# Performance work log

Measured on AMD Instinct MI355X. Metric: run time of the kernel, lower is better.

Reference implementation:

```python
import jax, jax.numpy as jnp
from jax import lax
import numpy as np

B, T, V, E, H, D, NH = 64, 121, 100000, 300, 256, 512, 3  # D = 2*H (BiLSTM output)


def setup_inputs() -> dict:
    key = jax.random.key(0)
    ks = jax.random.split(key, 24)
    s = 0.05
    n = lambda k, shp: (jax.random.normal(k, shp, dtype=jnp.float32) * s)
    return {
        'tokens': jax.random.randint(ks[0], (B, T), 0, V, dtype=jnp.int32),
        'lengths': jax.random.randint(ks[1], (B,), 1, T + 1, dtype=jnp.int32),
        'emb': n(ks[2], (V, E)),
        'Wx_f': n(ks[3], (E, 4 * H)), 'Wh_f': n(ks[4], (H, 4 * H)), 'b_f': jnp.zeros((4 * H,), jnp.float32),
        'Wx_b': n(ks[5], (E, 4 * H)), 'Wh_b': n(ks[6], (H, 4 * H)), 'b_b': jnp.zeros((4 * H,), jnp.float32),
        'W1': n(ks[7], (4 * D, E)), 'b1': jnp.zeros((E,), jnp.float32),
        'W2': n(ks[8], (E, 1)), 'b2': jnp.zeros((1,), jnp.float32),
        'Wr': n(ks[9], (D, D)), 'Ur': n(ks[10], (D, D)), 'br': jnp.zeros((D,), jnp.float32),
        'Wc': n(ks[11], (D, D)), 'Uc': n(ks[12], (D, D)), 'bc': jnp.zeros((D,), jnp.float32),
        'q': n(ks[13], (B, D)),
        'W_hops': n(ks[14], (NH, 3 * D, D)), 'b_hops': jnp.zeros((NH, D), jnp.float32),
        'Wo': n(ks[15], (2 * D, 1)), 'bo': jnp.zeros((1,), jnp.float32),
    }


def _lstm(x, Wx, Wh, b, reverse=False):
    # x: [B, T, E] -> outputs [B, T, H]
    xp = jnp.einsum('bte,eg->btg', x, Wx) + b  # precompute input projections
    def cell(carry, xt):
        h, c = carry
        g = xt + h @ Wh
        i, f, gg, o = jnp.split(g, 4, axis=-1)
        c = jax.nn.sigmoid(f) * c + jax.nn.sigmoid(i) * jnp.tanh(gg)
        h = jax.nn.sigmoid(o) * jnp.tanh(c)
        return (h, c), h
    h0 = jnp.zeros((x.shape[0], Wh.shape[0]), x.dtype)
    (_, _), ys = lax.scan(cell, (h0, h0), jnp.swapaxes(xp, 0, 1), reverse=reverse)
    return jnp.swapaxes(ys, 0, 1)


def _attention(facts, q, m, mask, W1, b1, W2, b2):
    # facts [B,T,D]; q,m [B,D] -> softmax attention [B,T] (masked by length)
    qe, me = q[:, None, :], m[:, None, :]
    z = jnp.concatenate([facts * qe, facts * me, jnp.abs(facts - qe), jnp.abs(facts - me)], axis=-1)
    h = jnp.tanh(jnp.einsum('btf,fe->bte', z, W1) + b1)
    s = (jnp.einsum('bte,eo->bto', h, W2) + b2)[..., 0]  # [B,T]
    s = jnp.where(mask, s, jnp.float32(-1e9))
    return jax.nn.softmax(s, axis=1)


def _attn_gru(facts, g, Wr, Ur, br, Wc, Uc, bc):
    # attention-gated GRU over time; episode = final state [B,D]
    def cell(h, inp):
        x, gt = inp
        r = jax.nn.sigmoid(x @ Wr + h @ Ur + br)
        hc = jnp.tanh(x @ Wc + r * (h @ Uc) + bc)
        h = gt[:, None] * hc + (1.0 - gt[:, None]) * h
        return h, None
    h0 = jnp.zeros_like(facts[:, 0])
    h, _ = lax.scan(cell, h0, (jnp.swapaxes(facts, 0, 1), g.T))
    return h


def reference(tokens, lengths, emb, Wx_f, Wh_f, b_f, Wx_b, Wh_b, b_b,
              W1, b1, W2, b2, Wr, Ur, br, Wc, Uc, bc, q,
              W_hops, b_hops, Wo, bo):
    x = emb[tokens]  # [B,T,E]
    fwd = _lstm(x, Wx_f, Wh_f, b_f, reverse=False)
    bwd = _lstm(x, Wx_b, Wh_b, b_b, reverse=True)
    facts = jnp.concatenate([fwd, bwd], axis=-1)  # [B,T,D]
    mask = jnp.arange(T)[None, :] < lengths[:, None]
    m = q
    for i in range(NH):  # episodic memory hops (attention weights shared across hops)
        a = _attention(facts, q, m, mask, W1, b1, W2, b2)
        ep = _attn_gru(facts, a, Wr, Ur, br, Wc, Uc, bc)
        m = jax.nn.relu(jnp.concatenate([m, ep, q], axis=1) @ W_hops[i] + b_hops[i])
    out = jax.nn.sigmoid(jnp.concatenate([m, q], axis=1) @ Wo + bo)
    return jnp.squeeze(out, axis=-1)  # [B]
```

## Files before the change

kernel.cpp:

```cpp
#include <hip/hip_runtime.h>

constexpr int B  = 64;
constexpr int T  = 121;
constexpr int E  = 300;
constexpr int Ep = 320;
constexpr int H  = 256;
constexpr int G4 = 1024;
constexpr int D  = 512;
constexpr int NH = 3;
constexpr int BT = B * T;
constexpr int Mp = 7808;

using short8 = __attribute__((ext_vector_type(8))) short;
using f32x4  = __attribute__((ext_vector_type(4))) float;

__device__ __forceinline__ float sigmoidf(float x) { return 1.0f / (1.0f + __expf(-x)); }
__device__ __forceinline__ float tanhf_fast(float x) {
  float e = __expf(2.0f * x);
  return 1.0f - 2.0f / (e + 1.0f);
}
__device__ __forceinline__ unsigned bf16rne(float x) {
  unsigned u = __float_as_uint(x);
  return (u + 0x7fffu + ((u >> 16) & 1u)) >> 16;
}
__device__ __forceinline__ float bf_lo(unsigned u) { return __uint_as_float(u << 16); }
__device__ __forceinline__ float bf_hi(unsigned u) { return __uint_as_float(u & 0xffff0000u); }
__device__ __forceinline__ float bfu(unsigned short u) { return __uint_as_float(((unsigned)u) << 16); }

#if defined(__has_builtin)
#if __has_builtin(__builtin_amdgcn_sdot4)
#define HAS_SDOT4 1
#endif
#if __has_builtin(__builtin_amdgcn_cvt_f32_ubyte0)
#define HAS_UBYTE 1
#endif
#endif
#ifdef HAS_UBYTE
__device__ __forceinline__ float UB0(unsigned u) { return __builtin_amdgcn_cvt_f32_ubyte0(u); }
__device__ __forceinline__ float UB1(unsigned u) { return __builtin_amdgcn_cvt_f32_ubyte1(u); }
__device__ __forceinline__ float UB2(unsigned u) { return __builtin_amdgcn_cvt_f32_ubyte2(u); }
__device__ __forceinline__ float UB3(unsigned u) { return __builtin_amdgcn_cvt_f32_ubyte3(u); }
#else
__device__ __forceinline__ float UB0(unsigned u) { return (float)(u & 0xffu); }
__device__ __forceinline__ float UB1(unsigned u) { return (float)((u >> 8) & 0xffu); }
__device__ __forceinline__ float UB2(unsigned u) { return (float)((u >> 16) & 0xffu); }
__device__ __forceinline__ float UB3(unsigned u) { return (float)((u >> 24) & 0xffu); }
#endif

__global__ void k_pack_lstm(const float* __restrict__ Wh,
                            uint4* __restrict__ PAQ, uint4* __restrict__ PBQ) {
  int idx = blockIdx.x * 256 + threadIdx.x;
  int k4 = idx >> 8, j = idx & 255;
  int k = 4 * k4;
  uint4 a, bq;
  const float* r0 = Wh + (size_t)(k + 0) * G4;
  const float* r1 = Wh + (size_t)(k + 1) * G4;
  const float* r2 = Wh + (size_t)(k + 2) * G4;
  const float* r3 = Wh + (size_t)(k + 3) * G4;
  a.x  = bf16rne(r0[j]) | (bf16rne(r0[j + 256]) << 16);
  a.y  = bf16rne(r1[j]) | (bf16rne(r1[j + 256]) << 16);
  a.z  = bf16rne(r2[j]) | (bf16rne(r2[j + 256]) << 16);
  a.w  = bf16rne(r3[j]) | (bf16rne(r3[j + 256]) << 16);
  bq.x = bf16rne(r0[j + 512]) | (bf16rne(r0[j + 768]) << 16);
  bq.y = bf16rne(r1[j + 512]) | (bf16rne(r1[j + 768]) << 16);
  bq.z = bf16rne(r2[j + 512]) | (bf16rne(r2[j + 768]) << 16);
  bq.w = bf16rne(r3[j + 512]) | (bf16rne(r3[j + 768]) << 16);
  PAQ[idx] = a;
  PBQ[idx] = bq;
}

__global__ void k_packT(const float* __restrict__ W, unsigned short* __restrict__ WT,
                        int Ksrc, int Nsrc, int stride, int Kpad) {
  int idx = blockIdx.x * 256 + threadIdx.x;
  int n = idx / Kpad, k = idx - n * Kpad;
  float v = (k < Ksrc && n < Nsrc) ? W[(size_t)k * stride + n] : 0.0f;
  WT[idx] = (unsigned short)bf16rne(v);
}

__global__ void k_packxrc(const float* xr, const float* xc, unsigned* XRC) {
  size_t i = (size_t)blockIdx.x * 512 + threadIdx.x;
  float r = xr[i], c = xc[i];
  XRC[i] = bf16rne(r) | (bf16rne(c) << 16);
}

__global__ void k_scales(const float* __restrict__ Ur, const float* __restrict__ Uc,
                         unsigned* __restrict__ smax) {
  int i = blockIdx.x * 256 + threadIdx.x;
  unsigned a = __float_as_uint(fabsf(Ur[i]));
  unsigned b = __float_as_uint(fabsf(Uc[i]));
  for (int off = 32; off > 0; off >>= 1) {
    a = max(a, (unsigned)__shfl_xor((int)a, off));
    b = max(b, (unsigned)__shfl_xor((int)b, off));
  }
  if ((threadIdx.x & 63) == 0) {
    atomicMax(&smax[0], a);
    atomicMax(&smax[1], b);
  }
}

#ifdef HAS_SDOT4
__device__ __forceinline__ unsigned pk4(float a, float b, float c, float d, float inv) {
  int qa = __float2int_rn(a * inv), qb = __float2int_rn(b * inv);
  int qc = __float2int_rn(c * inv), qd = __float2int_rn(d * inv);
  return (qa & 0xff) | ((qb & 0xff) << 8) | ((qc & 0xff) << 16) | ((qd & 0xff) << 24);
}
__global__ void k_pack_gru8(const float* __restrict__ Ur, const float* __restrict__ Uc,
                            const unsigned* __restrict__ smax, uint4* __restrict__ UQ8) {
  int idx = blockIdx.x * 256 + threadIdx.x;
  int k8 = idx >> 9, j = idx & 511;
  int k0 = k8 * 8;
  float invr = 127.0f / __uint_as_float(smax[0]);
  float invc = 127.0f / __uint_as_float(smax[1]);
  uint4 o;
  o.x = pk4(Ur[(size_t)(k0 + 0) * D + j], Ur[(size_t)(k0 + 1) * D + j],
            Ur[(size_t)(k0 + 2) * D + j], Ur[(size_t)(k0 + 3) * D + j], invr);
  o.y = pk4(Uc[(size_t)(k0 + 0) * D + j], Uc[(size_t)(k0 + 1) * D + j],
            Uc[(size_t)(k0 + 2) * D + j], Uc[(size_t)(k0 + 3) * D + j], invc);
  o.z = pk4(Ur[(size_t)(k0 + 4) * D + j], Ur[(size_t)(k0 + 5) * D + j],
            Ur[(size_t)(k0 + 6) * D + j], Ur[(size_t)(k0 + 7) * D + j], invr);
  o.w = pk4(Uc[(size_t)(k0 + 4) * D + j], Uc[(size_t)(k0 + 5) * D + j],
            Uc[(size_t)(k0 + 6) * D + j], Uc[(size_t)(k0 + 7) * D + j], invc);
  UQ8[idx] = o;
}
#else
__global__ void k_pack_gru8(const float* __restrict__ Ur, const float* __restrict__ Uc,
                            const unsigned* __restrict__ smax, uint4* __restrict__ UQ8) {
  int idx = blockIdx.x * 256 + threadIdx.x;
  int k8 = idx >> 9, j = idx & 511;
  float invr = 127.0f / __uint_as_float(smax[0]);
  float invc = 127.0f / __uint_as_float(smax[1]);
  unsigned dw[4];
#pragma unroll
  for (int d = 0; d < 4; ++d) {
    int k0 = k8 * 8 + 2 * d;
    unsigned r0 = (unsigned)(__float2int_rn(Ur[(size_t)k0 * D + j] * invr) + 128);
    unsigned c0 = (unsigned)(__float2int_rn(Uc[(size_t)k0 * D + j] * invc) + 128);
    unsigned r1 = (unsigned)(__float2int_rn(Ur[(size_t)(k0 + 1) * D + j] * invr) + 128);
    unsigned c1 = (unsigned)(__float2int_rn(Uc[(size_t)(k0 + 1) * D + j] * invc) + 128);
    dw[d] = r0 | (c0 << 8) | (r1 << 16) | (c1 << 24);
  }
  UQ8[idx] = make_uint4(dw[0], dw[1], dw[2], dw[3]);
}
#endif

__global__ void k_gather(const int* __restrict__ tokens, const float* __restrict__ emb,
                         unsigned short* __restrict__ xh) {
  int bt = blockIdx.x;
  int tok = tokens[bt];
  const float* src = emb + (size_t)tok * E;
  unsigned short* dst = xh + (size_t)bt * Ep;
  for (int e = threadIdx.x; e < Ep; e += 256)
    dst[e] = (e < E) ? (unsigned short)bf16rne(src[e]) : (unsigned short)0;
}

__global__ __launch_bounds__(256) void k_gemm_mfma(
    const unsigned short* __restrict__ A1, const unsigned short* __restrict__ B1, int K1, int lda1,
    const unsigned short* __restrict__ A2, const unsigned short* __restrict__ B2, int K2, int lda2,
    const float* __restrict__ bias, const float* __restrict__ Cin,
    float* __restrict__ C, int Nreal, int Cstride)
{
  __shared__ unsigned short As[128][40];
  __shared__ unsigned short Bs[64][40];
  int tid = threadIdx.x;
  int l = tid & 63, w = tid >> 6;
  int row0 = blockIdx.y * 128, col0 = blockIdx.x * 64;
  int lrow = l & 15, lk = (l >> 4) * 8, lq = (l >> 4) * 4;
  int ar = tid >> 1, asg = (tid & 1) * 16;
  int br = tid >> 2, bsg = (tid & 3) * 8;
  f32x4 acc[2][4] = {};
#pragma unroll 1
  for (int pass = 0; pass < 2; ++pass) {
    const unsigned short* A  = pass ? A2 : A1;
    const unsigned short* Bt = pass ? B2 : B1;
    int K   = pass ? K2 : K1;
    int lda = pass ? lda2 : lda1;
    if (K == 0) break;
    for (int k0 = 0; k0 < K; k0 += 32) {
      const uint4* ga = (const uint4*)(A + (size_t)(row0 + ar) * lda + k0 + asg);
      uint4 a0 = ga[0], a1 = ga[1];
      uint4 b0 = *(const uint4*)(Bt + (size_t)(col0 + br) * K + k0 + bsg);
      __syncthreads();
      *(uint4*)&As[ar][asg]     = a0;
      *(uint4*)&As[ar][asg + 8] = a1;
      *(uint4*)&Bs[br][bsg]     = b0;
      __syncthreads();
      short8 av[2], bv[4];
#pragma unroll
      for (int f = 0; f < 2; ++f)
        av[f] = *(const short8*)&As[w * 32 + f * 16 + lrow][lk];
#pragma unroll
      for (int fc = 0; fc < 4; ++fc)
        bv[fc] = *(const short8*)&Bs[fc * 16 + lrow][lk];
#pragma unroll
      for (int f = 0; f < 2; ++f)
#pragma unroll
        for (int fc = 0; fc < 4; ++fc)
          acc[f][fc] = __builtin_amdgcn_mfma_f32_16x16x32_bf16(av[f], bv[fc], acc[f][fc], 0, 0, 0);
    }
  }
#pragma unroll
  for (int f = 0; f < 2; ++f) {
#pragma unroll
    for (int fc = 0; fc < 4; ++fc) {
      int c = col0 + fc * 16 + lrow;
      if (c < Nreal) {
        float bb = bias ? bias[c] : 0.0f;
#pragma unroll
        for (int i = 0; i < 4; ++i) {
          int r = row0 + w * 32 + f * 16 + lq + i;
          if (r < BT) {
            float v = acc[f][fc][i] + bb;
            if (Cin) v += Cin[(size_t)r * Cstride + c];
            C[(size_t)r * Cstride + c] = v;
          }
        }
      }
    }
  }
}

__global__ __launch_bounds__(1024) void k_lstm(
    const float* __restrict__ xp_f, const float* __restrict__ xp_b,
    const uint4* __restrict__ PAQ_f, const uint4* __restrict__ PBQ_f,
    const uint4* __restrict__ PAQ_b, const uint4* __restrict__ PBQ_b,
    const int* __restrict__ lengths, unsigned short* __restrict__ factsh)
{
  int b = blockIdx.x;
  int dir = blockIdx.y;
  const float* xp = dir ? xp_b : xp_f;
  const uint4* PAQ = dir ? PAQ_b : PAQ_f;
  const uint4* PBQ = dir ? PBQ_b : PBQ_f;
  int tid = threadIdx.x;
  int j = tid & 255, quarter = tid >> 8;
  __shared__ float hs[H];
  __shared__ float4 red[1024];
  if (quarter == 0) hs[j] = 0.0f;
  float c = 0.0f, h = 0.0f;
  int nsteps = dir ? T : lengths[b];
  const uint4* pa = PAQ + (size_t)(quarter * 16) * 256 + j;
  const uint4* pb = PBQ + (size_t)(quarter * 16) * 256 + j;
  const float4* hs4 = reinterpret_cast<const float4*>(hs) + quarter * 16;
  __syncthreads();
  for (int s = 0; s < nsteps; ++s) {
    int t = dir ? (T - 1 - s) : s;
    float g0 = 0.f, g1 = 0.f, g2 = 0.f, g3 = 0.f;
#pragma unroll 4
    for (int k4 = 0; k4 < 16; ++k4) {
      uint4 a  = pa[(size_t)k4 * 256];
      uint4 bq = pb[(size_t)k4 * 256];
      float4 hv = hs4[k4];
      g0 = fmaf(hv.x, bf_lo(a.x), g0);  g1 = fmaf(hv.x, bf_hi(a.x), g1);
      g2 = fmaf(hv.x, bf_lo(bq.x), g2); g3 = fmaf(hv.x, bf_hi(bq.x), g3);
      g0 = fmaf(hv.y, bf_lo(a.y), g0);  g1 = fmaf(hv.y, bf_hi(a.y), g1);
      g2 = fmaf(hv.y, bf_lo(bq.y), g2); g3 = fmaf(hv.y, bf_hi(bq.y), g3);
      g0 = fmaf(hv.z, bf_lo(a.z), g0);  g1 = fmaf(hv.z, bf_hi(a.z), g1);
      g2 = fmaf(hv.z, bf_lo(bq.z), g2); g3 = fmaf(hv.z, bf_hi(bq.z), g3);
      g0 = fmaf(hv.w, bf_lo(a.w), g0);  g1 = fmaf(hv.w, bf_hi(a.w), g1);
      g2 = fmaf(hv.w, bf_lo(bq.w), g2); g3 = fmaf(hv.w, bf_hi(bq.w), g3);
    }
    red[tid] = make_float4(g0, g1, g2, g3);
    __syncthreads();
    if (quarter == 0) {
      float4 o1 = red[tid + 256];
      float4 o2 = red[tid + 512];
      float4 o3 = red[tid + 768];
      const float* xrow = xp + (size_t)(b * T + t) * G4;
      g0 += (o1.x + o2.x) + (o3.x + xrow[j]);
      g1 += (o1.y + o2.y) + (o3.y + xrow[j + 256]);
      g2 += (o1.z + o2.z) + (o3.z + xrow[j + 512]);
      g3 += (o1.w + o2.w) + (o3.w + xrow[j + 768]);
      float ig = sigmoidf(g0);
      float fg = sigmoidf(g1);
      float gg = tanhf_fast(g2);
      float og = sigmoidf(g3);
      c = fg * c + ig * gg;
      h = og * tanhf_fast(c);
      hs[j] = h;
      factsh[(size_t)(b * T + t) * D + dir * H + j] = (unsigned short)bf16rne(h);
    }
    __syncthreads();
  }
}

__global__ void k_buildz(const unsigned short* __restrict__ factsh, const float* __restrict__ v,
                         unsigned short* __restrict__ za, unsigned short* __restrict__ zb) {
  int bt = blockIdx.x;
  int b = bt / T;
  int d = threadIdx.x;
  float f = bfu(factsh[(size_t)bt * D + d]);
  float vv = v[(size_t)b * D + d];
  za[(size_t)bt * D + d] = (unsigned short)bf16rne(f * vv);
  zb[(size_t)bt * D + d] = (unsigned short)bf16rne(fabsf(f - vv));
}

__global__ void k_score(const float* __restrict__ att_h, const float* __restrict__ W2,
                        const float* __restrict__ b2, float* __restrict__ s) {
  int bt = blockIdx.x;
  int tid = threadIdx.x;
  float acc = 0.f;
  for (int e = tid; e < E; e += 64)
    acc += tanhf_fast(att_h[(size_t)bt * E + e]) * W2[e];
  for (int off = 32; off > 0; off >>= 1) acc += __shfl_down(acc, off);
  if (tid == 0) s[bt] = acc + b2[0];
}

__global__ void k_softmax(const float* __restrict__ s, const int* __restrict__ lengths,
                          float* __restrict__ a) {
  int b = blockIdx.x;
  int t = threadIdx.x;
  int len = lengths[b];
  __shared__ float wred[2];
  float val = -1e30f;
  if (t < T) val = (t < len) ? s[b * T + t] : -1e9f;
  float mx = val;
  for (int off = 32; off > 0; off >>= 1) mx = fmaxf(mx, __shfl_xor(mx, off));
  int wid = t >> 6, lane = t & 63;
  if (lane == 0) wred[wid] = mx;
  __syncthreads();
  mx = fmaxf(wred[0], wred[1]);
  __syncthreads();
  float e = (t < T && t < len) ? __expf(val - mx) : 0.0f;
  float sum = e;
  for (int off = 32; off > 0; off >>= 1) sum += __shfl_xor(sum, off);
  if (lane == 0) wred[wid] = sum;
  __syncthreads();
  float tot = wred[0] + wred[1];
  if (t < T) a[b * T + t] = e / tot;
}

__global__ void k_zero(int* __restrict__ p, int n) {
  int i = blockIdx.x * blockDim.x + threadIdx.x;
  if (i < n) p[i] = 0;
}

#ifdef HAS_SDOT4
__global__ __launch_bounds__(1024) void k_gru(
    const unsigned* __restrict__ XRC, const uint4* __restrict__ UQ8,
    const unsigned* __restrict__ smax,
    const float* __restrict__ br, const float* __restrict__ bc,
    const float* __restrict__ att, const int* __restrict__ lengths,
    float* __restrict__ ep)
{
  int b = blockIdx.x;
  int tid = threadIdx.x;
  int j = tid & 511, half = tid >> 9;
  __shared__ int hqs[D / 4];
  __shared__ int2 red2[1024];
  if (tid < D / 4) hqs[tid] = 0;
  float hj = 0.0f;
  int len = lengths[b];
  float sAr = __uint_as_float(smax[0]) * (1.0f / 16129.0f);
  float sAc = __uint_as_float(smax[1]) * (1.0f / 16129.0f);
  float brj = br[j], bcj = bc[j];
  const uint4* up = UQ8 + (size_t)(half * 32) * 512 + j;
  __syncthreads();
  for (int t = 0; t < len; ++t) {
    float g = att[b * T + t];
    unsigned xq = XRC[(size_t)(b * T + t) * D + j];
    int ar = 0, ac = 0;
#pragma unroll 8
    for (int k8 = 0; k8 < 32; ++k8) {
      uint4 u = up[(size_t)k8 * 512];
      int h0 = hqs[(half * 32 + k8) * 2];
      int h1 = hqs[(half * 32 + k8) * 2 + 1];
      ar = __builtin_amdgcn_sdot4(h0, (int)u.x, ar, false);
      ac = __builtin_amdgcn_sdot4(h0, (int)u.y, ac, false);
      ar = __builtin_amdgcn_sdot4(h1, (int)u.z, ar, false);
      ac = __builtin_amdgcn_sdot4(h1, (int)u.w, ac, false);
    }
    red2[tid] = make_int2(ar, ac);
    __syncthreads();
    if (half == 0) {
      int2 o = red2[tid + 512];
      float racc = sAr * (float)(ar + o.x);
      float cacc = sAc * (float)(ac + o.y);
      float r  = sigmoidf(bf_lo(xq) + racc + brj);
      float hc = tanhf_fast(bf_hi(xq) + r * cacc + bcj);
      hj = g * hc + (1.f - g) * hj;
      ((signed char*)hqs)[j] = (signed char)__float2int_rn(hj * 127.0f);
    }
    __syncthreads();
  }
  if (half == 0) ep[(size_t)b * D + j] = hj;
}
#else
__global__ __launch_bounds__(1024) void k_gru(
    const unsigned* __restrict__ XRC, const uint4* __restrict__ UQ8,
    const unsigned* __restrict__ smax,
    const float* __restrict__ br, const float* __restrict__ bc,
    const float* __restrict__ att, const int* __restrict__ lengths,
    float* __restrict__ ep)
{
  int b = blockIdx.x;
  int tid = threadIdx.x;
  int j = tid & 511, half = tid >> 9;
  __shared__ float hs[D];
  __shared__ float2 red[1024];
  __shared__ float hsL;
  if (half == 0) hs[j] = 0.0f;
  if (tid == 0) hsL = 0.0f;
  float hj = 0.0f;
  int len = lengths[b];
  float s_r = __uint_as_float(smax[0]) * (1.0f / 127.0f);
  float s_c = __uint_as_float(smax[1]) * (1.0f / 127.0f);
  float brj = br[j], bcj = bc[j];
  const uint4* up = UQ8 + (size_t)(half * 32) * 512 + j;
  const float4* hs4 = reinterpret_cast<const float4*>(hs);
  __syncthreads();
  for (int t = 0; t < len; ++t) {
    float g = att[b * T + t];
    unsigned xq = XRC[(size_t)(b * T + t) * D + j];
    float qr = 0.f, qc = 0.f;
#pragma unroll 8
    for (int k8 = 0; k8 < 32; ++k8) {
      uint4 u = up[(size_t)k8 * 512];
      float4 h0 = hs4[(half * 32 + k8) * 2];
      float4 h1 = hs4[(half * 32 + k8) * 2 + 1];
      qr = fmaf(h0.x, UB0(u.x), qr); qc = fmaf(h0.x, UB1(u.x), qc);
      qr = fmaf(h0.y, UB2(u.x), qr); qc = fmaf(h0.y, UB3(u.x), qc);
      qr = fmaf(h0.z, UB0(u.y), qr); qc = fmaf(h0.z, UB1(u.y), qc);
      qr = fmaf(h0.w, UB2(u.y), qr); qc = fmaf(h0.w, UB3(u.y), qc);
      qr = fmaf(h1.x, UB0(u.z), qr); qc = fmaf(h1.x, UB1(u.z), qc);
      qr = fmaf(h1.y, UB2(u.z), qr); qc = fmaf(h1.y, UB3(u.z), qc);
      qr = fmaf(h1.z, UB0(u.w), qr); qc = fmaf(h1.z, UB1(u.w), qc);
      qr = fmaf(h1.w, UB2(u.w), qr); qc = fmaf(h1.w, UB3(u.w), qc);
    }
    red[tid] = make_float2(qr, qc);
    __syncthreads();
    if (half == 0) {
      float2 o = red[tid + 512];
      float hsum = hsL;
      float racc = s_r * (qr + o.x - 128.0f * hsum);
      float cacc = s_c * (qc + o.y - 128.0f * hsum);
      float r  = sigmoidf(bf_lo(xq) + racc + brj);
      float hc = tanhf_fast(bf_hi(xq) + r * cacc + bcj);
      hj = g * hc + (1.f - g) * hj;
      hs[j] = hj;
    }
    __syncthreads();
    if (tid < 64) {
      float4 a = hs4[2 * tid], bq = hs4[2 * tid + 1];
      float s4 = ((a.x + a.y) + (a.z + a.w)) + ((bq.x + bq.y) + (bq.z + bq.w));
      for (int off = 32; off > 0; off >>= 1) s4 += __shfl_down(s4, off);
      if (tid == 0) hsL = s4;
    }
  }
  if (half == 0) ep[(size_t)b * D + j] = hj;
}
#endif

__global__ __launch_bounds__(512) void k_hop(
    const float* __restrict__ m_in, const float* __restrict__ ep,
    const float* __restrict__ q, const float* __restrict__ Whop,
    const float* __restrict__ bhop, float* __restrict__ m_out)
{
  int b = blockIdx.x, j = threadIdx.x;
  __shared__ float av[3 * D];
  av[j]         = m_in[(size_t)b * D + j];
  av[D + j]     = ep[(size_t)b * D + j];
  av[2 * D + j] = q[(size_t)b * D + j];
  __syncthreads();
  float acc = bhop[j];
#pragma unroll 4
  for (int k = 0; k < 3 * D; ++k)
    acc = fmaf(av[k], Whop[(size_t)k * D + j], acc);
  m_out[(size_t)b * D + j] = fmaxf(acc, 0.0f);
}

__global__ void k_out(const float* __restrict__ m, const float* __restrict__ q,
                      const float* __restrict__ Wo, const float* __restrict__ bo,
                      float* __restrict__ out)
{
  int b = blockIdx.x, tid = threadIdx.x;
  float acc = 0.f;
  for (int k = tid; k < D; k += 256)
    acc += m[(size_t)b * D + k] * Wo[k] + q[(size_t)b * D + k] * Wo[D + k];
  for (int off = 32; off > 0; off >>= 1) acc += __shfl_down(acc, off);
  __shared__ float red[4];
  int wid = tid >> 6, lane = tid & 63;
  if (lane == 0) red[wid] = acc;
  __syncthreads();
  if (tid == 0) {
    float tot = red[0] + red[1] + red[2] + red[3];
    out[b] = 1.0f / (1.0f + __expf(-(tot + bo[0])));
  }
}

extern "C" void kernel_launch(void* const* d_in, const int* in_sizes, int n_in,
                              void* d_out, int out_size, void* d_ws, size_t ws_size,
                              hipStream_t stream)
{
  const int*   tokens  = (const int*)d_in[0];
  const int*   lengths = (const int*)d_in[1];
  const float* emb     = (const float*)d_in[2];
  const float* Wx_f    = (const float*)d_in[3];
  const float* Wh_f    = (const float*)d_in[4];
  const float* b_f     = (const float*)d_in[5];
  const float* Wx_b    = (const float*)d_in[6];
  const float* Wh_b    = (const float*)d_in[7];
  const float* b_b     = (const float*)d_in[8];
  const float* W1      = (const float*)d_in[9];
  const float* b1      = (const float*)d_in[10];
  const float* W2      = (const float*)d_in[11];
  const float* b2      = (const float*)d_in[12];
  const float* Wr      = (const float*)d_in[13];
  const float* Ur      = (const float*)d_in[14];
  const float* br      = (const float*)d_in[15];
  const float* Wc      = (const float*)d_in[16];
  const float* Uc      = (const float*)d_in[17];
  const float* bc      = (const float*)d_in[18];
  const float* q       = (const float*)d_in[19];
  const float* W_hops  = (const float*)d_in[20];
  const float* b_hops  = (const float*)d_in[21];
  const float* Wo      = (const float*)d_in[22];
  const float* bo      = (const float*)d_in[23];
  float* ws = (float*)d_ws;

  float* p = ws;
  unsigned short* xh = (unsigned short*)p;  p += (size_t)Mp * Ep / 2;
  float* xp_f   = p;  p += (size_t)BT * G4;
  float* xp_b   = p;  p += (size_t)BT * G4;
  unsigned short* factsh = (unsigned short*)p;  p += (size_t)Mp * D / 2;
  float* att_h  = p;  p += (size_t)BT * E;
  float* part0  = p;  p += (size_t)BT * E;
  float* scores = p;  p += BT;
  float* att    = p;  p += BT;
  float* m0     = p;  p += (size_t)B * D;
  float* m1     = p;  p += (size_t)B * D;
  float* epb    = p;  p += (size_t)B * D;
  unsigned* smax = (unsigned*)p;  p += 4;
  uint4* UQ8    = (uint4*)p;  p += (size_t)(D / 8) * D * 4;
  uint4* PAQ_f  = (uint4*)p;  p += (size_t)(H / 4) * 256 * 4;
  uint4* PBQ_f  = (uint4*)p;  p += (size_t)(H / 4) * 256 * 4;
  uint4* PAQ_b  = (uint4*)p;  p += (size_t)(H / 4) * 256 * 4;
  uint4* PBQ_b  = (uint4*)p;  p += (size_t)(H / 4) * 256 * 4;
  unsigned short* WxT_f = (unsigned short*)p;  p += (size_t)G4 * Ep / 2;
  unsigned short* WxT_b = (unsigned short*)p;  p += (size_t)G4 * Ep / 2;
  unsigned short* WrT   = (unsigned short*)p;  p += (size_t)D * D / 2;
  unsigned short* WcT   = (unsigned short*)p;  p += (size_t)D * D / 2;
  unsigned short* W1T[4];
  for (int c = 0; c < 4; ++c) { W1T[c] = (unsigned short*)p; p += (size_t)Ep * D / 2; }
  float* xr = xp_f;
  float* xc = xp_f + (size_t)BT * D;
  unsigned* XRC = (unsigned*)xr;
  unsigned short* za = (unsigned short*)xp_b;
  unsigned short* zb = (unsigned short*)xp_b + (size_t)Mp * D;

  k_zero<<<1, 64, 0, stream>>>((int*)smax, 4);
  k_scales<<<D * D / 256, 256, 0, stream>>>(Ur, Uc, smax);
  k_pack_gru8<<<(D / 8) * D / 256, 256, 0, stream>>>(Ur, Uc, smax, UQ8);
  k_pack_lstm<<<(H / 4) * 256 / 256, 256, 0, stream>>>(Wh_f, PAQ_f, PBQ_f);
  k_pack_lstm<<<(H / 4) * 256 / 256, 256, 0, stream>>>(Wh_b, PAQ_b, PBQ_b);
  k_packT<<<G4 * Ep / 256, 256, 0, stream>>>(Wx_f, WxT_f, E, G4, G4, Ep);
  k_packT<<<G4 * Ep / 256, 256, 0, stream>>>(Wx_b, WxT_b, E, G4, G4, Ep);
  k_packT<<<D * D / 256, 256, 0, stream>>>(Wr, WrT, D, D, D, D);
  k_packT<<<D * D / 256, 256, 0, stream>>>(Wc, WcT, D, D, D, D);
  for (int c = 0; c < 4; ++c)
    k_packT<<<Ep * D / 256, 256, 0, stream>>>(W1 + (size_t)c * D * E, W1T[c], D, E, E, D);

  k_gather<<<BT, 256, 0, stream>>>(tokens, emb, xh);
  k_gemm_mfma<<<dim3(G4 / 64, Mp / 128), 256, 0, stream>>>(
      xh, WxT_f, Ep, Ep, nullptr, nullptr, 0, 0, b_f, nullptr, xp_f, G4, G4);
  k_gemm_mfma<<<dim3(G4 / 64, Mp / 128), 256, 0, stream>>>(
      xh, WxT_b, Ep, Ep, nullptr, nullptr, 0, 0, b_b, nullptr, xp_b, G4, G4);
  k_lstm<<<dim3(B, 2), 1024, 0, stream>>>(xp_f, xp_b, PAQ_f, PBQ_f, PAQ_b, PBQ_b, lengths, factsh);
  k_gemm_mfma<<<dim3(D / 64, Mp / 128), 256, 0, stream>>>(
      factsh, WrT, D, D, nullptr, nullptr, 0, 0, nullptr, nullptr, xr, D, D);
  k_gemm_mfma<<<dim3(D / 64, Mp / 128), 256, 0, stream>>>(
      factsh, WcT, D, D, nullptr, nullptr, 0, 0, nullptr, nullptr, xc, D, D);
  k_packxrc<<<BT * D / 512, 512, 0, stream>>>(xr, xc, XRC);
  k_buildz<<<BT, 512, 0, stream>>>(factsh, q, za, zb);
  k_gemm_mfma<<<dim3(Ep / 64, Mp / 128), 256, 0, stream>>>(
      za, W1T[0], D, D, zb, W1T[2], D, D, b1, nullptr, part0, E, E);

  const float* m_in = q;
  float* mb[2] = {m0, m1};
  for (int i = 0; i < NH; ++i) {
    k_buildz<<<BT, 512, 0, stream>>>(factsh, m_in, za, zb);
    k_gemm_mfma<<<dim3(Ep / 64, Mp / 128), 256, 0, stream>>>(
        za, W1T[1], D, D, zb, W1T[3], D, D, nullptr, part0, att_h, E, E);
    k_score<<<BT, 64, 0, stream>>>(att_h, W2, b2, scores);
    k_softmax<<<B, 128, 0, stream>>>(scores, lengths, att);
    k_gru<<<B, 1024, 0, stream>>>(XRC, UQ8, smax, br, bc, att, lengths, epb);
    k_hop<<<B, 512, 0, stream>>>(m_in, epb, q,
                                 W_hops + (size_t)i * 3 * D * D, b_hops + (size_t)i * D,
                                 mb[i & 1]);
    m_in = mb[i & 1];
  }
  k_out<<<B, 256, 0, stream>>>(m_in, q, Wo, bo, (float*)d_out);
}
```

Measured before the change: 2.803 ms.

## Quantize LSTM recurrent weights to offset uint8 with per-matrix scale

```diff
diff --git a/kernel.cpp b/kernel.cpp
--- a/kernel.cpp
+++ b/kernel.cpp
@@ -47,28 +47,6 @@
 __device__ __forceinline__ float UB3(unsigned u) { return (float)((u >> 24) & 0xffu); }
 #endif
 
-__global__ void k_pack_lstm(const float* __restrict__ Wh,
-                            uint4* __restrict__ PAQ, uint4* __restrict__ PBQ) {
-  int idx = blockIdx.x * 256 + threadIdx.x;
-  int k4 = idx >> 8, j = idx & 255;
-  int k = 4 * k4;
-  uint4 a, bq;
-  const float* r0 = Wh + (size_t)(k + 0) * G4;
-  const float* r1 = Wh + (size_t)(k + 1) * G4;
-  const float* r2 = Wh + (size_t)(k + 2) * G4;
-  const float* r3 = Wh + (size_t)(k + 3) * G4;
-  a.x  = bf16rne(r0[j]) | (bf16rne(r0[j + 256]) << 16);
-  a.y  = bf16rne(r1[j]) | (bf16rne(r1[j + 256]) << 16);
-  a.z  = bf16rne(r2[j]) | (bf16rne(r2[j + 256]) << 16);
-  a.w  = bf16rne(r3[j]) | (bf16rne(r3[j + 256]) << 16);
-  bq.x = bf16rne(r0[j + 512]) | (bf16rne(r0[j + 768]) << 16);
-  bq.y = bf16rne(r1[j + 512]) | (bf16rne(r1[j + 768]) << 16);
-  bq.z = bf16rne(r2[j + 512]) | (bf16rne(r2[j + 768]) << 16);
-  bq.w = bf16rne(r3[j + 512]) | (bf16rne(r3[j + 768]) << 16);
-  PAQ[idx] = a;
-  PBQ[idx] = bq;
-}
-
 __global__ void k_packT(const float* __restrict__ W, unsigned short* __restrict__ WT,
                         int Ksrc, int Nsrc, int stride, int Kpad) {
   int idx = blockIdx.x * 256 + threadIdx.x;
@@ -96,6 +74,32 @@
     atomicMax(&smax[0], a);
     atomicMax(&smax[1], b);
   }
+}
+
+__global__ void k_scalesW(const float* __restrict__ W, unsigned* __restrict__ out) {
+  int i = blockIdx.x * 256 + threadIdx.x;
+  unsigned a = __float_as_uint(fabsf(W[i]));
+  for (int off = 32; off > 0; off >>= 1)
+    a = max(a, (unsigned)__shfl_xor((int)a, off));
+  if ((threadIdx.x & 63) == 0) atomicMax(&out[0], a);
+}
+
+__global__ void k_pack_lstm_u8(const float* __restrict__ Wh,
+                               const unsigned* __restrict__ sW, uint4* __restrict__ PU8) {
+  int idx = blockIdx.x * 256 + threadIdx.x;
+  int k4 = idx >> 8, j = idx & 255;
+  float inv = 127.0f / __uint_as_float(sW[0]);
+  unsigned dw[4];
+#pragma unroll
+  for (int d = 0; d < 4; ++d) {
+    const float* row = Wh + (size_t)(4 * k4 + d) * G4;
+    unsigned qi = (unsigned)(__float2int_rn(row[j]       * inv) + 128);
+    unsigned qf = (unsigned)(__float2int_rn(row[j + 256] * inv) + 128);
+    unsigned qg = (unsigned)(__float2int_rn(row[j + 512] * inv) + 128);
+    unsigned qo = (unsigned)(__float2int_rn(row[j + 768] * inv) + 128);
+    dw[d] = qi | (qf << 8) | (qg << 16) | (qo << 24);
+  }
+  PU8[idx] = make_uint4(dw[0], dw[1], dw[2], dw[3]);
 }
 
 #ifdef HAS_SDOT4
@@ -221,42 +225,43 @@
 
 __global__ __launch_bounds__(1024) void k_lstm(
     const float* __restrict__ xp_f, const float* __restrict__ xp_b,
-    const uint4* __restrict__ PAQ_f, const uint4* __restrict__ PBQ_f,
-    const uint4* __restrict__ PAQ_b, const uint4* __restrict__ PBQ_b,
+    const uint4* __restrict__ PU8_f, const uint4* __restrict__ PU8_b,
+    const unsigned* __restrict__ smax,
     const int* __restrict__ lengths, unsigned short* __restrict__ factsh)
 {
   int b = blockIdx.x;
   int dir = blockIdx.y;
   const float* xp = dir ? xp_b : xp_f;
-  const uint4* PAQ = dir ? PAQ_b : PAQ_f;
-  const uint4* PBQ = dir ? PBQ_b : PBQ_f;
+  const uint4* PU = dir ? PU8_b : PU8_f;
   int tid = threadIdx.x;
   int j = tid & 255, quarter = tid >> 8;
   __shared__ float hs[H];
   __shared__ float4 red[1024];
+  __shared__ float hsL;
   if (quarter == 0) hs[j] = 0.0f;
+  if (tid == 0) hsL = 0.0f;
   float c = 0.0f, h = 0.0f;
   int nsteps = dir ? T : lengths[b];
-  const uint4* pa = PAQ + (size_t)(quarter * 16) * 256 + j;
-  const uint4* pb = PBQ + (size_t)(quarter * 16) * 256 + j;
-  const float4* hs4 = reinterpret_cast<const float4*>(hs) + quarter * 16;
+  float sW = __uint_as_float(smax[2 + dir]) * (1.0f / 127.0f);
+  const uint4* pu = PU + (size_t)(quarter * 16) * 256 + j;
+  const float4* hs4q = reinterpret_cast<const float4*>(hs) + quarter * 16;
+  const float4* hs4  = reinterpret_cast<const float4*>(hs);
   __syncthreads();
   for (int s = 0; s < nsteps; ++s) {
     int t = dir ? (T - 1 - s) : s;
     float g0 = 0.f, g1 = 0.f, g2 = 0.f, g3 = 0.f;
 #pragma unroll 4
     for (int k4 = 0; k4 < 16; ++k4) {
-      uint4 a  = pa[(size_t)k4 * 256];
-      uint4 bq = pb[(size_t)k4 * 256];
-      float4 hv = hs4[k4];
-      g0 = fmaf(hv.x, bf_lo(a.x), g0);  g1 = fmaf(hv.x, bf_hi(a.x), g1);
-      g2 = fmaf(hv.x, bf_lo(bq.x), g2); g3 = fmaf(hv.x, bf_hi(bq.x), g3);
-      g0 = fmaf(hv.y, bf_lo(a.y), g0);  g1 = fmaf(hv.y, bf_hi(a.y), g1);
-      g2 = fmaf(hv.y, bf_lo(bq.y), g2); g3 = fmaf(hv.y, bf_hi(bq.y), g3);
-      g0 = fmaf(hv.z, bf_lo(a.z), g0);  g1 = fmaf(hv.z, bf_hi(a.z), g1);
-      g2 = fmaf(hv.z, bf_lo(bq.z), g2); g3 = fmaf(hv.z, bf_hi(bq.z), g3);
-      g0 = fmaf(hv.w, bf_lo(a.w), g0);  g1 = fmaf(hv.w, bf_hi(a.w), g1);
-      g2 = fmaf(hv.w, bf_lo(bq.w), g2); g3 = fmaf(hv.w, bf_hi(bq.w), g3);
+      uint4 u = pu[(size_t)k4 * 256];
+      float4 hv = hs4q[k4];
+      g0 = fmaf(hv.x, UB0(u.x), g0); g1 = fmaf(hv.x, UB1(u.x), g1);
+      g2 = fmaf(hv.x, UB2(u.x), g2); g3 = fmaf(hv.x, UB3(u.x), g3);
+      g0 = fmaf(hv.y, UB0(u.y), g0); g1 = fmaf(hv.y, UB1(u.y), g1);
+      g2 = fmaf(hv.y, UB2(u.y), g2); g3 = fmaf(hv.y, UB3(u.y), g3);
+      g0 = fmaf(hv.z, UB0(u.z), g0); g1 = fmaf(hv.z, UB1(u.z), g1);
+      g2 = fmaf(hv.z, UB2(u.z), g2); g3 = fmaf(hv.z, UB3(u.z), g3);
+      g0 = fmaf(hv.w, UB0(u.w), g0); g1 = fmaf(hv.w, UB1(u.w), g1);
+      g2 = fmaf(hv.w, UB2(u.w), g2); g3 = fmaf(hv.w, UB3(u.w), g3);
     }
     red[tid] = make_float4(g0, g1, g2, g3);
     __syncthreads();
@@ -264,21 +269,32 @@
       float4 o1 = red[tid + 256];
       float4 o2 = red[tid + 512];
       float4 o3 = red[tid + 768];
+      float hsum = hsL;
       const float* xrow = xp + (size_t)(b * T + t) * G4;
-      g0 += (o1.x + o2.x) + (o3.x + xrow[j]);
-      g1 += (o1.y + o2.y) + (o3.y + xrow[j + 256]);
-      g2 += (o1.z + o2.z) + (o3.z + xrow[j + 512]);
-      g3 += (o1.w + o2.w) + (o3.w + xrow[j + 768]);
-      float ig = sigmoidf(g0);
-      float fg = sigmoidf(g1);
-      float gg = tanhf_fast(g2);
-      float og = sigmoidf(g3);
+      float q0 = g0 + (o1.x + o2.x) + o3.x;
+      float q1 = g1 + (o1.y + o2.y) + o3.y;
+      float q2 = g2 + (o1.z + o2.z) + o3.z;
+      float q3 = g3 + (o1.w + o2.w) + o3.w;
+      float a0 = xrow[j]       + sW * (q0 - 128.0f * hsum);
+      float a1 = xrow[j + 256] + sW * (q1 - 128.0f * hsum);
+      float a2 = xrow[j + 512] + sW * (q2 - 128.0f * hsum);
+      float a3 = xrow[j + 768] + sW * (q3 - 128.0f * hsum);
+      float ig = sigmoidf(a0);
+      float fg = sigmoidf(a1);
+      float gg = tanhf_fast(a2);
+      float og = sigmoidf(a3);
       c = fg * c + ig * gg;
       h = og * tanhf_fast(c);
       hs[j] = h;
       factsh[(size_t)(b * T + t) * D + dir * H + j] = (unsigned short)bf16rne(h);
     }
     __syncthreads();
+    if (tid < 64) {
+      float4 a = hs4[tid];
+      float s4 = (a.x + a.y) + (a.z + a.w);
+      for (int off = 32; off > 0; off >>= 1) s4 += __shfl_down(s4, off);
+      if (tid == 0) hsL = s4;
+    }
   }
 }
 
@@ -530,10 +546,11 @@
   float* epb    = p;  p += (size_t)B * D;
   unsigned* smax = (unsigned*)p;  p += 4;
   uint4* UQ8    = (uint4*)p;  p += (size_t)(D / 8) * D * 4;
-  uint4* PAQ_f  = (uint4*)p;  p += (size_t)(H / 4) * 256 * 4;
-  uint4* PBQ_f  = (uint4*)p;  p += (size_t)(H / 4) * 256 * 4;
-  uint4* PAQ_b  = (uint4*)p;  p += (size_t)(H / 4) * 256 * 4;
-  uint4* PBQ_b  = (uint4*)p;  p += (size_t)(H / 4) * 256 * 4;
+  uint4* PU8_f  = (uint4*)p;  p += (size_t)(H / 4) * 256 * 4;
+  uint4* PU8_b  = (uint4*)p;  p += (size_t)(H / 4) * 256 * 4;
+  uint4* unused0 = (uint4*)p;  p += (size_t)(H / 4) * 256 * 4;
+  uint4* unused1 = (uint4*)p;  p += (size_t)(H / 4) * 256 * 4;
+  (void)unused0; (void)unused1;
   unsigned short* WxT_f = (unsigned short*)p;  p += (size_t)G4 * Ep / 2;
   unsigned short* WxT_b = (unsigned short*)p;  p += (size_t)G4 * Ep / 2;
   unsigned short* WrT   = (unsigned short*)p;  p += (size_t)D * D / 2;
@@ -548,9 +565,11 @@
 
   k_zero<<<1, 64, 0, stream>>>((int*)smax, 4);
   k_scales<<<D * D / 256, 256, 0, stream>>>(Ur, Uc, smax);
+  k_scalesW<<<H * G4 / 256, 256, 0, stream>>>(Wh_f, smax + 2);
+  k_scalesW<<<H * G4 / 256, 256, 0, stream>>>(Wh_b, smax + 3);
   k_pack_gru8<<<(D / 8) * D / 256, 256, 0, stream>>>(Ur, Uc, smax, UQ8);
-  k_pack_lstm<<<(H / 4) * 256 / 256, 256, 0, stream>>>(Wh_f, PAQ_f, PBQ_f);
-  k_pack_lstm<<<(H / 4) * 256 / 256, 256, 0, stream>>>(Wh_b, PAQ_b, PBQ_b);
+  k_pack_lstm_u8<<<(H / 4) * 256 / 256, 256, 0, stream>>>(Wh_f, smax + 2, PU8_f);
+  k_pack_lstm_u8<<<(H / 4) * 256 / 256, 256, 0, stream>>>(Wh_b, smax + 3, PU8_b);
   k_packT<<<G4 * Ep / 256, 256, 0, stream>>>(Wx_f, WxT_f, E, G4, G4, Ep);
   k_packT<<<G4 * Ep / 256, 256, 0, stream>>>(Wx_b, WxT_b, E, G4, G4, Ep);
   k_packT<<<D * D / 256, 256, 0, stream>>>(Wr, WrT, D, D, D, D);
@@ -563,7 +582,7 @@
       xh, WxT_f, Ep, Ep, nullptr, nullptr, 0, 0, b_f, nullptr, xp_f, G4, G4);
   k_gemm_mfma<<<dim3(G4 / 64, Mp / 128), 256, 0, stream>>>(
       xh, WxT_b, Ep, Ep, nullptr, nullptr, 0, 0, b_b, nullptr, xp_b, G4, G4);
-  k_lstm<<<dim3(B, 2), 1024, 0, stream>>>(xp_f, xp_b, PAQ_f, PBQ_f, PAQ_b, PBQ_b, lengths, factsh);
+  k_lstm<<<dim3(B, 2), 1024, 0, stream>>>(xp_f, xp_b, PU8_f, PU8_b, smax, lengths, factsh);
   k_gemm_mfma<<<dim3(D / 64, Mp / 128), 256, 0, stream>>>(
       factsh, WrT, D, D, nullptr, nullptr, 0, 0, nullptr, nullptr, xr, D, D);
   k_gemm_mfma<<<dim3(D / 64, Mp / 128), 256, 0, stream>>>(
```

Result: no change. 2.794 ms (-0.3%).
